# Kernel optimization log

Measured on AMD Instinct MI355X. Metric: run time of the kernel, lower is better.

Reference implementation:

```python
import jax, jax.numpy as jnp
import numpy as np
import math

# Static config (matches init_kwargs / input_specs)
SPATIAL = [(64, 64), (32, 32), (16, 16), (8, 8)]  # (H_l, W_l)
BN, LQ, C, M, L, P = 2, 4000, 256, 8, 4, 4
D = C // M  # 32, dim per head


def _bilinear_sample(vflat, H, W, loc):
    """grid_sample(mode=bilinear, padding=zeros, align_corners=False).
    vflat: [N, H*W, M, D]; loc: [N, Lq, M, P, 2] normalized in [0,1].
    Returns [N, Lq, M, P, D].
    Note: grid = 2*loc-1, then x = (g+1)*W/2 - 0.5 == loc*W - 0.5."""
    x = loc[..., 0] * W - 0.5
    y = loc[..., 1] * H - 0.5
    x0f = jnp.floor(x)
    y0f = jnp.floor(y)
    tx = x - x0f
    ty = y - y0f
    x0 = x0f.astype(jnp.int32)
    y0 = y0f.astype(jnp.int32)
    nidx = jnp.arange(vflat.shape[0])[:, None, None, None]
    midx = jnp.arange(vflat.shape[2])[None, None, :, None]
    out = jnp.zeros(loc.shape[:-1] + (vflat.shape[-1],), vflat.dtype)
    for dx, dy, w in ((0, 0, (1 - tx) * (1 - ty)), (1, 0, tx * (1 - ty)),
                      (0, 1, (1 - tx) * ty), (1, 1, tx * ty)):
        xi = x0 + dx
        yi = y0 + dy
        valid = (xi >= 0) & (xi < W) & (yi >= 0) & (yi < H)
        xc = jnp.clip(xi, 0, W - 1)
        yc = jnp.clip(yi, 0, H - 1)
        g = vflat[nidx, yc * W + xc, midx]  # [N,Lq,M,P,D]
        out = out + (w * valid)[..., None] * g
    return out


def setup_inputs() -> dict:
    key = jax.random.key(0)
    ks = jax.random.split(key, 16)
    Lin = sum(h * w for h, w in SPATIAL)
    s = 0.02
    inp = {
        'query': jax.random.normal(ks[0], (BN, LQ, C), jnp.float32),
        'reference_points': jax.random.uniform(ks[1], (BN, LQ, L, 2), jnp.float32),
        'input_flatten': jax.random.normal(ks[2], (BN, Lin, C), jnp.float32),
        'input_spatial_shapes': jnp.array(SPATIAL, jnp.int32),
        'input_level_start_index': jnp.array(
            np.cumsum([0] + [h * w for h, w in SPATIAL[:-1]]), jnp.int32),
        'Wv': jax.random.normal(ks[3], (C, C), jnp.float32) * s,
        'bv': jnp.zeros((C,), jnp.float32),
        'Wk': jax.random.normal(ks[4], (C, C), jnp.float32) * s,
        'bk': jnp.zeros((C,), jnp.float32),
        'Wq': jax.random.normal(ks[5], (C, C), jnp.float32) * s,
        'bq': jnp.zeros((C,), jnp.float32),
        'Woff': jax.random.normal(ks[6], (C, M * L * P * 2), jnp.float32) * s,
        'boff': jax.random.normal(ks[7], (M * L * P * 2,), jnp.float32) * 0.5,
        'Wout': jax.random.normal(ks[8], (C, C), jnp.float32) * s,
        'bout': jnp.zeros((C,), jnp.float32),
    }
    return inp


def _forward(query, reference_points, input_flatten,
             Wv, bv, Wk, bk, Wq, bq, Woff, boff, Wout, bout):
    N, Lq, _ = query.shape
    Lin = input_flatten.shape[1]
    value = (input_flatten @ Wv + bv).reshape(N, Lin, M, D)
    keyf = (input_flatten @ Wk + bk).reshape(N, Lin, M, D)
    q = (query @ Wq + bq).reshape(N, Lq, M, D)
    # sampling locations: ref + offsets / [W_l, H_l]
    off = (query @ Woff + boff).reshape(N, Lq, M, L, P, 2)
    norm = jnp.array([[w, h] for h, w in SPATIAL], jnp.float32)  # [L,2]
    loc = reference_points[:, :, None, :, None, :] + off / norm[None, None, None, :, None, :]
    sk_list, sv_list = [], []
    start = 0
    for lid, (H, W) in enumerate(SPATIAL):
        vl = value[:, start:start + H * W]   # [N,HW,M,D]
        kl = keyf[:, start:start + H * W]
        loc_l = loc[:, :, :, lid]            # [N,Lq,M,P,2]
        sv_list.append(_bilinear_sample(vl, H, W, loc_l))
        sk_list.append(_bilinear_sample(kl, H, W, loc_l))
        start += H * W
    sk = jnp.stack(sk_list, axis=3)  # [N,Lq,M,L,P,D]
    sv = jnp.stack(sv_list, axis=3)
    # key-aware attention: per-query softmax over the L*P sampled keys
    logits = jnp.einsum('nqmd,nqmlpd->nqmlp', q, sk) / math.sqrt(D)
    attn = jax.nn.softmax(logits.reshape(N, Lq, M, L * P), axis=-1)
    out = jnp.einsum('nqmk,nqmkd->nqmd', attn, sv.reshape(N, Lq, M, L * P, D))
    out = out.reshape(N, Lq, C) @ Wout + bout
    return out


def reference(query, reference_points, input_flatten, input_spatial_shapes,
              input_level_start_index, Wv, bv, Wk, bk, Wq, bq, Woff, boff,
              Wout, bout):
    return _forward(query, reference_points, input_flatten,
                    Wv, bv, Wk, bk, Wq, bq, Woff, boff, Wout, bout)
```

## Files before the change

kernel.cpp:

```cpp
#include <hip/hip_runtime.h>

#define NB   2
#define LQN  4000
#define CC   256
#define LIN  5440
#define ROWS1 (NB * LIN)
#define ROWS2 (NB * LQN)
#define ELEMS1 (ROWS1 * CC)

typedef short bf16x8 __attribute__((ext_vector_type(8)));
typedef float f32x4 __attribute__((ext_vector_type(4)));

__device__ __forceinline__ unsigned short f2b(float f) {
    union { float f; unsigned u; } v; v.f = f;
    unsigned r = v.u + 0x7FFFu + ((v.u >> 16) & 1u);
    return (unsigned short)(r >> 16);
}
__device__ __forceinline__ float b2f(unsigned short u) {
    union { unsigned u; float f; } v; v.u = ((unsigned)u) << 16; return v.f;
}

__global__ __launch_bounds__(256) void prep(
    const float* __restrict__ xflat, const float* __restrict__ query,
    const float* __restrict__ Wv, const float* __restrict__ Wk,
    const float* __restrict__ Wq, const float* __restrict__ Wo,
    const float* __restrict__ Wout,
    unsigned short* __restrict__ Ab, unsigned short* __restrict__ WT)
{
    const int bx = blockIdx.x, tid = threadIdx.x;
    if (bx < 2360) {
        const size_t e = (size_t)bx * 2048 + (size_t)tid * 8;
        const float* src = (e < ELEMS1) ? xflat + e : query + (e - ELEMS1);
        float4 a = *(const float4*)src;
        float4 b = *(const float4*)(src + 4);
        bf16x8 o;
        o[0] = (short)f2b(a.x); o[1] = (short)f2b(a.y);
        o[2] = (short)f2b(a.z); o[3] = (short)f2b(a.w);
        o[4] = (short)f2b(b.x); o[5] = (short)f2b(b.y);
        o[6] = (short)f2b(b.z); o[7] = (short)f2b(b.w);
        *(bf16x8*)&Ab[e] = o;
    } else {
        const int b2 = bx - 2360;
        const int mat = b2 >> 8, n = b2 & 255, k = tid;
        const float* W = (mat == 0) ? Wv : (mat == 1) ? Wk : (mat == 2) ? Wq
                       : (mat == 3) ? Wo : Wout;
        WT[mat * 65536 + n * 256 + k] = f2b(W[k * 256 + n]);
    }
}

__global__ __launch_bounds__(256) void gemm_pw(
    const unsigned short* __restrict__ Ab,
    const unsigned short* __restrict__ WT,
    const float* __restrict__ bv, const float* __restrict__ bk,
    const float* __restrict__ bq, const float* __restrict__ bo,
    unsigned short* __restrict__ value, unsigned short* __restrict__ keyf,
    float* __restrict__ qproj, float* __restrict__ offp)
{
    const int bx = blockIdx.x;
    const int tid = threadIdx.x;
    const int w = tid >> 6, lane = tid & 63;
    const int m16 = lane & 15, q4 = lane >> 4;
    const bool isA1 = bx < (ROWS1 / 16);
    const int mat = (isA1 ? 0 : 2) + (w >> 1);
    const int col0 = (w & 1) * 128;

    const unsigned short* Ap = Ab + (size_t)bx * (16 * 256) + m16 * 256 + q4 * 8;
    const unsigned short* Bp = WT + (size_t)mat * 65536 + (size_t)(col0 + m16) * 256 + q4 * 8;

    f32x4 acc[8];
    #pragma unroll
    for (int j = 0; j < 8; ++j) acc[j] = (f32x4){0.f, 0.f, 0.f, 0.f};

    bf16x8 aC, bC[8], aN, bN[8];
    aC = *(const bf16x8*)Ap;
    #pragma unroll
    for (int ct = 0; ct < 8; ++ct)
        bC[ct] = *(const bf16x8*)(Bp + ct * (16 * 256));

    #pragma unroll
    for (int kt = 0; kt < 8; ++kt) {
        if (kt < 7) {
            const int k1 = (kt + 1) * 32;
            aN = *(const bf16x8*)(Ap + k1);
            #pragma unroll
            for (int ct = 0; ct < 8; ++ct)
                bN[ct] = *(const bf16x8*)(Bp + ct * (16 * 256) + k1);
        }
        #pragma unroll
        for (int ct = 0; ct < 8; ++ct)
            acc[ct] = __builtin_amdgcn_mfma_f32_16x16x32_bf16(aC, bC[ct], acc[ct], 0, 0, 0);
        if (kt < 7) {
            aC = aN;
            #pragma unroll
            for (int ct = 0; ct < 8; ++ct) bC[ct] = bN[ct];
        }
    }

    const int row0l = (isA1 ? bx : bx - ROWS1 / 16) * 16;
    if (mat <= 1) {
        unsigned short* C = mat ? keyf : value;
        const float* bias = mat ? bk : bv;
        #pragma unroll
        for (int ct = 0; ct < 8; ++ct) {
            const int col = col0 + ct * 16 + m16;
            const float bcol = bias[col];
            #pragma unroll
            for (int e = 0; e < 4; ++e) {
                const int r = row0l + q4 * 4 + e;
                C[(size_t)r * 256 + col] = f2b(acc[ct][e] + bcol);
            }
        }
    } else {
        float* C = (mat == 3) ? offp : qproj;
        const float* bias = (mat == 3) ? bo : bq;
        #pragma unroll
        for (int ct = 0; ct < 8; ++ct) {
            const int col = col0 + ct * 16 + m16;
            const float bcol = bias[col];
            #pragma unroll
            for (int e = 0; e < 4; ++e) {
                const int r = row0l + q4 * 4 + e;
                C[(size_t)r * 256 + col] = acc[ct][e] + bcol;
            }
        }
    }
}

__global__ __launch_bounds__(512) void gemm_outm(
    const unsigned short* __restrict__ Am,
    const unsigned short* __restrict__ WoT,
    const float* __restrict__ bias, float* __restrict__ C)
{
    const int bx = blockIdx.x;
    const int tid = threadIdx.x;
    const int w = tid >> 6, lane = tid & 63;
    const int m16 = lane & 15, q4 = lane >> 4;
    const int col0 = w * 32;

    const unsigned short* Ap = Am + (size_t)bx * (16 * 256) + m16 * 256 + q4 * 8;
    const unsigned short* Bp = WoT + (size_t)(col0 + m16) * 256 + q4 * 8;

    f32x4 acc[2];
    acc[0] = (f32x4){0.f, 0.f, 0.f, 0.f};
    acc[1] = (f32x4){0.f, 0.f, 0.f, 0.f};

    bf16x8 aC, bC[2], aN, bN[2];
    aC = *(const bf16x8*)Ap;
    bC[0] = *(const bf16x8*)Bp;
    bC[1] = *(const bf16x8*)(Bp + 16 * 256);

    #pragma unroll
    for (int kt = 0; kt < 8; ++kt) {
        if (kt < 7) {
            const int k1 = (kt + 1) * 32;
            aN = *(const bf16x8*)(Ap + k1);
            bN[0] = *(const bf16x8*)(Bp + k1);
            bN[1] = *(const bf16x8*)(Bp + 16 * 256 + k1);
        }
        acc[0] = __builtin_amdgcn_mfma_f32_16x16x32_bf16(aC, bC[0], acc[0], 0, 0, 0);
        acc[1] = __builtin_amdgcn_mfma_f32_16x16x32_bf16(aC, bC[1], acc[1], 0, 0, 0);
        if (kt < 7) { aC = aN; bC[0] = bN[0]; bC[1] = bN[1]; }
    }

    #pragma unroll
    for (int ct = 0; ct < 2; ++ct) {
        const int col = col0 + ct * 16 + m16;
        const float bcol = bias[col];
        #pragma unroll
        for (int e = 0; e < 4; ++e) {
            const int r = bx * 16 + q4 * 4 + e;
            C[(size_t)r * 256 + col] = acc[ct][e] + bcol;
        }
    }
}

__global__ __launch_bounds__(256) void sample_attn(
    const float* __restrict__ qproj,
    const float* __restrict__ offp,
    const float* __restrict__ refp,
    const unsigned short* __restrict__ value,
    const unsigned short* __restrict__ keyf,
    unsigned short* __restrict__ outmid)
{
    const int bx = blockIdx.x;
    const int n = bx / LQN;
    const int tid = threadIdx.x;

    __shared__ float s_off[256];
    __shared__ float s_ref[8];
    __shared__ __align__(16) float s_w[8][16][4];
    __shared__ __align__(16) int   s_idx[8][16][4];

    const int baseq = bx * CC;
    s_off[tid] = offp[baseq + tid];
    if (tid < 8) s_ref[tid] = refp[bx * 8 + tid];
    __syncthreads();

    if (tid < 128) {
        const int pm = tid >> 4, l = (tid >> 2) & 3, p = tid & 3;
        const int HW = 64 >> l;
        const int st = (l == 0) ? 0 : (l == 1) ? 4096 : (l == 2) ? 5120 : 5376;
        const float fHW = (float)HW;
        float x = s_ref[l * 2 + 0] * fHW + s_off[pm * 32 + l * 8 + p * 2 + 0] - 0.5f;
        float y = s_ref[l * 2 + 1] * fHW + s_off[pm * 32 + l * 8 + p * 2 + 1] - 0.5f;
        float x0f = floorf(x), y0f = floorf(y);
        float txf = x - x0f, tyf = y - y0f;
        int x0 = (int)x0f, y0 = (int)y0f;
        int x1 = x0 + 1, y1 = y0 + 1;
        float fx0 = (x0 >= 0 && x0 < HW) ? (1.f - txf) : 0.f;
        float fx1 = (x1 >= 0 && x1 < HW) ? txf : 0.f;
        float fy0 = (y0 >= 0 && y0 < HW) ? (1.f - tyf) : 0.f;
        float fy1 = (y1 >= 0 && y1 < HW) ? tyf : 0.f;
        int xc0 = min(max(x0, 0), HW - 1), xc1 = min(max(x1, 0), HW - 1);
        int yc0 = min(max(y0, 0), HW - 1), yc1 = min(max(y1, 0), HW - 1);
        const int pt = l * 4 + p;
        s_w[pm][pt][0] = fx0 * fy0;
        s_w[pm][pt][1] = fx1 * fy0;
        s_w[pm][pt][2] = fx0 * fy1;
        s_w[pm][pt][3] = fx1 * fy1;
        const int eb = pm * 32;
        s_idx[pm][pt][0] = (st + yc0 * HW + xc0) * CC + eb;
        s_idx[pm][pt][1] = (st + yc0 * HW + xc1) * CC + eb;
        s_idx[pm][pt][2] = (st + yc1 * HW + xc0) * CC + eb;
        s_idx[pm][pt][3] = (st + yc1 * HW + xc1) * CC + eb;
    }
    __syncthreads();

    const int m = tid >> 5, lane = tid & 31;
    const int p2 = lane >> 3, dq = lane & 7;
    const size_t nbase = (size_t)n * LIN * CC;
    const unsigned short* vbp = value + nbase;
    const unsigned short* kbp = keyf + nbase;
    const int doff = dq * 4;

    const float4 q4 = *(const float4*)&qproj[baseq + m * 32 + doff];

    float lg[4];
    float4 vv[4];

    #pragma unroll
    for (int r = 0; r < 4; ++r) {
        const int pt = r * 4 + p2;
        float4 w4 = *(const float4*)&s_w[m][pt][0];
        int4  i4 = *(const int4*)&s_idx[m][pt][0];
        ushort4 ka = *(const ushort4*)(kbp + i4.x + doff);
        ushort4 kb = *(const ushort4*)(kbp + i4.y + doff);
        ushort4 kc = *(const ushort4*)(kbp + i4.z + doff);
        ushort4 kd = *(const ushort4*)(kbp + i4.w + doff);
        ushort4 va = *(const ushort4*)(vbp + i4.x + doff);
        ushort4 vb = *(const ushort4*)(vbp + i4.y + doff);
        ushort4 vc = *(const ushort4*)(vbp + i4.z + doff);
        ushort4 vd = *(const ushort4*)(vbp + i4.w + doff);
        float4 ks;
        ks.x = fmaf(w4.w, b2f(kd.x), fmaf(w4.z, b2f(kc.x), fmaf(w4.y, b2f(kb.x), w4.x * b2f(ka.x))));
        ks.y = fmaf(w4.w, b2f(kd.y), fmaf(w4.z, b2f(kc.y), fmaf(w4.y, b2f(kb.y), w4.x * b2f(ka.y))));
        ks.z = fmaf(w4.w, b2f(kd.z), fmaf(w4.z, b2f(kc.z), fmaf(w4.y, b2f(kb.z), w4.x * b2f(ka.z))));
        ks.w = fmaf(w4.w, b2f(kd.w), fmaf(w4.z, b2f(kc.w), fmaf(w4.y, b2f(kb.w), w4.x * b2f(ka.w))));
        vv[r].x = fmaf(w4.w, b2f(vd.x), fmaf(w4.z, b2f(vc.x), fmaf(w4.y, b2f(vb.x), w4.x * b2f(va.x))));
        vv[r].y = fmaf(w4.w, b2f(vd.y), fmaf(w4.z, b2f(vc.y), fmaf(w4.y, b2f(vb.y), w4.x * b2f(va.y))));
        vv[r].z = fmaf(w4.w, b2f(vd.z), fmaf(w4.z, b2f(vc.z), fmaf(w4.y, b2f(vb.z), w4.x * b2f(va.z))));
        vv[r].w = fmaf(w4.w, b2f(vd.w), fmaf(w4.z, b2f(vc.w), fmaf(w4.y, b2f(vb.w), w4.x * b2f(va.w))));
        float s = fmaf(q4.w, ks.w, fmaf(q4.z, ks.z, fmaf(q4.y, ks.y, q4.x * ks.x)));
        s += __shfl_xor(s, 1);
        s += __shfl_xor(s, 2);
        s += __shfl_xor(s, 4);
        lg[r] = s * 0.17677669529663687f;
    }

    float mx = fmaxf(fmaxf(lg[0], lg[1]), fmaxf(lg[2], lg[3]));
    mx = fmaxf(mx, __shfl_xor(mx, 8));
    mx = fmaxf(mx, __shfl_xor(mx, 16));
    float e0 = __expf(lg[0] - mx), e1 = __expf(lg[1] - mx);
    float e2 = __expf(lg[2] - mx), e3 = __expf(lg[3] - mx);
    float Z = e0 + e1 + e2 + e3;
    Z += __shfl_xor(Z, 8);
    Z += __shfl_xor(Z, 16);

    float4 o;
    o.x = fmaf(e3, vv[3].x, fmaf(e2, vv[2].x, fmaf(e1, vv[1].x, e0 * vv[0].x)));
    o.y = fmaf(e3, vv[3].y, fmaf(e2, vv[2].y, fmaf(e1, vv[1].y, e0 * vv[0].y)));
    o.z = fmaf(e3, vv[3].z, fmaf(e2, vv[2].z, fmaf(e1, vv[1].z, e0 * vv[0].z)));
    o.w = fmaf(e3, vv[3].w, fmaf(e2, vv[2].w, fmaf(e1, vv[1].w, e0 * vv[0].w)));
    #pragma unroll
    for (int msk = 8; msk <= 16; msk <<= 1) {
        o.x += __shfl_xor(o.x, msk);
        o.y += __shfl_xor(o.y, msk);
        o.z += __shfl_xor(o.z, msk);
        o.w += __shfl_xor(o.w, msk);
    }
    if (p2 == 0) {
        const float rz = 1.0f / Z;
        ushort4 res = make_ushort4(f2b(o.x * rz), f2b(o.y * rz),
                                   f2b(o.z * rz), f2b(o.w * rz));
        *(ushort4*)&outmid[baseq + m * 32 + doff] = res;
    }
}

extern "C" void kernel_launch(void* const* d_in, const int* in_sizes, int n_in,
                              void* d_out, int out_size, void* d_ws, size_t ws_size,
                              hipStream_t stream) {
    const float* query = (const float*)d_in[0];
    const float* refp  = (const float*)d_in[1];
    const float* xflat = (const float*)d_in[2];
    const float* Wv   = (const float*)d_in[5];
    const float* bv   = (const float*)d_in[6];
    const float* Wk   = (const float*)d_in[7];
    const float* bk   = (const float*)d_in[8];
    const float* Wq   = (const float*)d_in[9];
    const float* bq   = (const float*)d_in[10];
    const float* Woff = (const float*)d_in[11];
    const float* boff = (const float*)d_in[12];
    const float* Wout = (const float*)d_in[13];
    const float* bout = (const float*)d_in[14];

    char* ws = (char*)d_ws;
    unsigned short* value  = (unsigned short*)ws; ws += (size_t)ROWS1 * CC * 2;
    unsigned short* keyf   = (unsigned short*)ws; ws += (size_t)ROWS1 * CC * 2;
    float* qproj  = (float*)ws; ws += (size_t)ROWS2 * CC * 4;
    float* offp   = (float*)ws; ws += (size_t)ROWS2 * CC * 4;
    unsigned short* outmid = (unsigned short*)ws; ws += (size_t)ROWS2 * CC * 2;
    unsigned short* Ab = (unsigned short*)ws; ws += (size_t)(ROWS1 + ROWS2) * CC * 2;
    unsigned short* WT = (unsigned short*)ws; ws += 5 * 65536 * 2;

    dim3 blk(256);

    prep<<<dim3(2360 + 1280), blk, 0, stream>>>(xflat, query, Wv, Wk, Wq, Woff, Wout, Ab, WT);

    gemm_pw<<<dim3(ROWS1 / 16 + ROWS2 / 16), blk, 0, stream>>>(
        Ab, WT, bv, bk, bq, boff, value, keyf, qproj, offp);

    sample_attn<<<dim3(NB * LQN), blk, 0, stream>>>(qproj, offp, refp, value, keyf, outmid);

    gemm_outm<<<dim3(ROWS2 / 16), dim3(512), 0, stream>>>(
        outmid, WT + 4 * 65536, bout, (float*)d_out);
}
```

Baseline: 188.7 us.

## Retile projection GEMM into 64x256 blocks per matrix for register reuse

The projection GEMM is reorganised so each block computes a 64-row by 256-column tile of one weight matrix, with each wave holding a 4x4 grid of MFMA accumulators instead of a 16-row strip across eight column tiles. This reuses each loaded A and B fragment four times in registers, which cuts global/L2 load traffic per MFMA. The grid becomes 590 blocks instead of 1180, so there is less parallelism and more register pressure per thread.

```diff
diff --git a/kernel.cpp b/kernel.cpp
--- a/kernel.cpp
+++ b/kernel.cpp
@@ -60,68 +60,78 @@
     const int tid = threadIdx.x;
     const int w = tid >> 6, lane = tid & 63;
     const int m16 = lane & 15, q4 = lane >> 4;
-    const bool isA1 = bx < (ROWS1 / 16);
-    const int mat = (isA1 ? 0 : 2) + (w >> 1);
-    const int col0 = (w & 1) * 128;
-
-    const unsigned short* Ap = Ab + (size_t)bx * (16 * 256) + m16 * 256 + q4 * 8;
-    const unsigned short* Bp = WT + (size_t)mat * 65536 + (size_t)(col0 + m16) * 256 + q4 * 8;
-
-    f32x4 acc[8];
-    #pragma unroll
-    for (int j = 0; j < 8; ++j) acc[j] = (f32x4){0.f, 0.f, 0.f, 0.f};
-
-    bf16x8 aC, bC[8], aN, bN[8];
-    aC = *(const bf16x8*)Ap;
-    #pragma unroll
-    for (int ct = 0; ct < 8; ++ct)
-        bC[ct] = *(const bf16x8*)(Bp + ct * (16 * 256));
+
+    int mat, rowTile, rowBase;
+    if (bx < 340) { mat = bx & 1; rowTile = bx >> 1; rowBase = rowTile * 64; }
+    else { const int b2 = bx - 340; mat = 2 + (b2 & 1); rowTile = b2 >> 1; rowBase = ROWS1 + rowTile * 64; }
+
+    const unsigned short* Ap = Ab + (size_t)(rowBase + m16) * 256 + q4 * 8;
+    const unsigned short* Bp = WT + (size_t)mat * 65536 + (size_t)(w * 64 + m16) * 256 + q4 * 8;
+
+    f32x4 acc[4][4];
+    #pragma unroll
+    for (int i = 0; i < 4; ++i)
+        #pragma unroll
+        for (int j = 0; j < 4; ++j) acc[i][j] = (f32x4){0.f, 0.f, 0.f, 0.f};
+
+    bf16x8 aC[4], bC[4], aN[4], bN[4];
+    #pragma unroll
+    for (int rt = 0; rt < 4; ++rt) aC[rt] = *(const bf16x8*)(Ap + rt * (16 * 256));
+    #pragma unroll
+    for (int ct = 0; ct < 4; ++ct) bC[ct] = *(const bf16x8*)(Bp + ct * (16 * 256));
 
     #pragma unroll
     for (int kt = 0; kt < 8; ++kt) {
         if (kt < 7) {
             const int k1 = (kt + 1) * 32;
-            aN = *(const bf16x8*)(Ap + k1);
-            #pragma unroll
-            for (int ct = 0; ct < 8; ++ct)
-                bN[ct] = *(const bf16x8*)(Bp + ct * (16 * 256) + k1);
-        }
-        #pragma unroll
-        for (int ct = 0; ct < 8; ++ct)
-            acc[ct] = __builtin_amdgcn_mfma_f32_16x16x32_bf16(aC, bC[ct], acc[ct], 0, 0, 0);
+            #pragma unroll
+            for (int rt = 0; rt < 4; ++rt) aN[rt] = *(const bf16x8*)(Ap + rt * (16 * 256) + k1);
+            #pragma unroll
+            for (int ct = 0; ct < 4; ++ct) bN[ct] = *(const bf16x8*)(Bp + ct * (16 * 256) + k1);
+        }
+        #pragma unroll
+        for (int rt = 0; rt < 4; ++rt)
+            #pragma unroll
+            for (int ct = 0; ct < 4; ++ct)
+                acc[rt][ct] = __builtin_amdgcn_mfma_f32_16x16x32_bf16(aC[rt], bC[ct], acc[rt][ct], 0, 0, 0);
         if (kt < 7) {
-            aC = aN;
-            #pragma unroll
-            for (int ct = 0; ct < 8; ++ct) bC[ct] = bN[ct];
-        }
-    }
-
-    const int row0l = (isA1 ? bx : bx - ROWS1 / 16) * 16;
+            #pragma unroll
+            for (int rt = 0; rt < 4; ++rt) aC[rt] = aN[rt];
+            #pragma unroll
+            for (int ct = 0; ct < 4; ++ct) bC[ct] = bN[ct];
+        }
+    }
+
+    const int row0l = rowTile * 64;
     if (mat <= 1) {
         unsigned short* C = mat ? keyf : value;
         const float* bias = mat ? bk : bv;
         #pragma unroll
-        for (int ct = 0; ct < 8; ++ct) {
-            const int col = col0 + ct * 16 + m16;
+        for (int ct = 0; ct < 4; ++ct) {
+            const int col = w * 64 + ct * 16 + m16;
             const float bcol = bias[col];
             #pragma unroll
-            for (int e = 0; e < 4; ++e) {
-                const int r = row0l + q4 * 4 + e;
-                C[(size_t)r * 256 + col] = f2b(acc[ct][e] + bcol);
-            }
+            for (int rt = 0; rt < 4; ++rt)
+                #pragma unroll
+                for (int e = 0; e < 4; ++e) {
+                    const int r = row0l + rt * 16 + q4 * 4 + e;
+                    C[(size_t)r * 256 + col] = f2b(acc[rt][ct][e] + bcol);
+                }
         }
     } else {
         float* C = (mat == 3) ? offp : qproj;
         const float* bias = (mat == 3) ? bo : bq;
         #pragma unroll
-        for (int ct = 0; ct < 8; ++ct) {
-            const int col = col0 + ct * 16 + m16;
+        for (int ct = 0; ct < 4; ++ct) {
+            const int col = w * 64 + ct * 16 + m16;
             const float bcol = bias[col];
             #pragma unroll
-            for (int e = 0; e < 4; ++e) {
-                const int r = row0l + q4 * 4 + e;
-                C[(size_t)r * 256 + col] = acc[ct][e] + bcol;
-            }
+            for (int rt = 0; rt < 4; ++rt)
+                #pragma unroll
+                for (int e = 0; e < 4; ++e) {
+                    const int r = row0l + rt * 16 + q4 * 4 + e;
+                    C[(size_t)r * 256 + col] = acc[rt][ct][e] + bcol;
+                }
         }
     }
 }
@@ -326,7 +336,7 @@
 
     prep<<<dim3(2360 + 1280), blk, 0, stream>>>(xflat, query, Wv, Wk, Wq, Woff, Wout, Ab, WT);
 
-    gemm_pw<<<dim3(ROWS1 / 16 + ROWS2 / 16), blk, 0, stream>>>(
+    gemm_pw<<<dim3(340 + 250), blk, 0, stream>>>(
         Ab, WT, bv, bk, bq, boff, value, keyf, qproj, offp);
 
     sample_attn<<<dim3(NB * LQN), blk, 0, stream>>>(qproj, offp, refp, value, keyf, outmid);
```

Result: faster. 171.8 us (-9.0%).
